# Kernel tuning notes

Hardware: AMD Instinct MI355X
Metric: run time of the kernel (lower is better)

## Reference

```python
import jax, jax.numpy as jnp
import numpy as np

B, TK, H = 32, 1024, 512
N = 2 * H          # hidden_dim * 2
AD = 512           # attention_dimension


def setup_inputs() -> dict:
    key = jax.random.key(0)
    ks = jax.random.split(key, 11)
    s = 0.02  # weight scale
    return {
        's_t_hat': jax.random.normal(ks[0], (B, N), jnp.float32),
        'encoder_outputs': jax.random.normal(ks[1], (B, TK, N), jnp.float32),
        'encoder_feature': jax.random.normal(ks[2], (B * TK, N), jnp.float32),
        'enc_padding_mask': jax.random.uniform(ks[3], (B, TK), jnp.float32),
        'coverage': jax.random.uniform(ks[4], (B, TK), jnp.float32),
        'r_i': jax.random.normal(ks[5], (B, TK, AD), jnp.float32),
        'W_s_w': jax.random.normal(ks[6], (N, N), jnp.float32) * s,
        'W_s_b': jax.random.normal(ks[7], (N,), jnp.float32) * s,
        'W_c_w': jax.random.normal(ks[8], (N, 1), jnp.float32) * s,
        'v_w': jax.random.normal(ks[9], (1, N), jnp.float32) * s,
        'W_r_w': jax.random.normal(ks[10], (N, AD), jnp.float32) * s,
    }


def reference(s_t_hat, encoder_outputs, encoder_feature, enc_padding_mask,
              coverage, r_i, W_s_w, W_s_b, W_c_w, v_w, W_r_w):
    b, t_k, n = encoder_outputs.shape
    # decoder feature: W_s(s_t_hat), broadcast over time
    dec_fea = s_t_hat @ W_s_w.T + W_s_b                       # [b, n]
    enc_feat = encoder_feature.reshape(b, t_k, n)             # [b, t_k, n]
    # coverage feature: W_c applied to scalar coverage per position
    cov_feat = coverage[..., None] * W_c_w[:, 0]              # [b, t_k, n]
    e = jnp.tanh(enc_feat + dec_fea[:, None, :] + cov_feat)   # [b, t_k, n]
    scores = jnp.einsum('btn,n->bt', e, v_w[0])               # [b, t_k]
    attn_ = jax.nn.softmax(scores, axis=1) * enc_padding_mask
    attn = attn_ / attn_.sum(1, keepdims=True)                # renormalized
    c_t = jnp.einsum('bt,btn->bn', attn, encoder_outputs)     # [b, n]
    coverage_new = coverage + attn                            # [b, t_k]
    # structural (LSA) branch
    Wrri = jnp.einsum('bta,na->btn', r_i, W_r_w)              # [b, t_k, n]
    e_s = jnp.tanh(Wrri + dec_fea[:, None, :])
    s2 = jnp.einsum('btn,n->bt', e_s, v_w[0])
    a_struct = (jax.nn.softmax(s2, axis=1) * enc_padding_mask)[:, None, :]  # [b,1,t_k]
    c_t_struct = jnp.einsum('bt,btn->bn', a_struct[:, 0], encoder_outputs)  # [b, n]
    return (c_t, attn, coverage_new, c_t_struct, a_struct)
```

## Files before the change

### kernel.cpp

```cpp
#include <hip/hip_runtime.h>
#include <hip/hip_bf16.h>

static constexpr int BB   = 32;
static constexpr int TKK  = 1024;
static constexpr int ND   = 1024;
static constexpr int ADIM = 512;

typedef __attribute__((ext_vector_type(8))) short bf16x8;
typedef __attribute__((ext_vector_type(4))) float f32x4;

__device__ __forceinline__ float fast_tanh(float x) {
  x = fminf(fmaxf(x, -15.f), 15.f);
  float e = __expf(2.f * x);
  return __fdividef(e - 1.f, e + 1.f);
}

__device__ __forceinline__ short f2bf(float x) {
  unsigned u = __float_as_uint(x);
  u += 0x7FFF + ((u >> 16) & 1);
  return (short)(u >> 16);
}

__device__ __forceinline__ void gload_lds16(const void* g, void* l) {
  __builtin_amdgcn_global_load_lds(
      (const __attribute__((address_space(1))) unsigned int*)g,
      (__attribute__((address_space(3))) unsigned int*)l, 16, 0, 0);
}

__global__ __launch_bounds__(256) void k_cvt2(const float* __restrict__ r_i,
    const float* __restrict__ Wr, short* __restrict__ rb, short* __restrict__ wb) {
  size_t bid = blockIdx.x;
  const float* src;
  short* dst;
  size_t i;
  if (bid < 8192) { src = r_i; dst = rb; i = bid * 256 + threadIdx.x; }
  else            { src = Wr;  dst = wb; i = (bid - 8192) * 256 + threadIdx.x; }
  float4 a = ((const float4*)src)[2 * i];
  float4 b = ((const float4*)src)[2 * i + 1];
  bf16x8 h;
  h[0] = f2bf(a.x); h[1] = f2bf(a.y); h[2] = f2bf(a.z); h[3] = f2bf(a.w);
  h[4] = f2bf(b.x); h[5] = f2bf(b.y); h[6] = f2bf(b.z); h[7] = f2bf(b.w);
  ((bf16x8*)dst)[i] = h;
}

__global__ __launch_bounds__(256) void k_decfea(const float* __restrict__ s_t_hat,
    const float* __restrict__ Wsw, const float* __restrict__ Wsb,
    float* __restrict__ dec) {
  int b  = blockIdx.x >> 3;
  int n0 = (blockIdx.x & 7) << 7;
  int w = threadIdx.x >> 6, lane = threadIdx.x & 63;
  const float4* s4 = (const float4*)(s_t_hat + (size_t)b * ND);
  float4 sv0 = s4[lane], sv1 = s4[lane + 64], sv2 = s4[lane + 128], sv3 = s4[lane + 192];
  for (int nn = 0; nn < 32; nn++) {
    int n = n0 + w * 32 + nn;
    const float4* w4 = (const float4*)(Wsw + (size_t)n * ND);
    float4 wa = w4[lane], wb = w4[lane + 64], wc = w4[lane + 128], wd = w4[lane + 192];
    float acc = sv0.x*wa.x + sv0.y*wa.y + sv0.z*wa.z + sv0.w*wa.w
              + sv1.x*wb.x + sv1.y*wb.y + sv1.z*wb.z + sv1.w*wb.w
              + sv2.x*wc.x + sv2.y*wc.y + sv2.z*wc.z + sv2.w*wc.w
              + sv3.x*wd.x + sv3.y*wd.y + sv3.z*wd.z + sv3.w*wd.w;
    #pragma unroll
    for (int off = 32; off; off >>= 1) acc += __shfl_down(acc, off);
    if (lane == 0) dec[b * ND + n] = acc + Wsb[n];
  }
}

__global__ __launch_bounds__(256) void k_scoresA(const float* __restrict__ ef,
    const float* __restrict__ dec, const float* __restrict__ Wc,
    const float* __restrict__ vw, const float* __restrict__ cov,
    float* __restrict__ scores) {
  const int bt = blockIdx.x * 4 + (threadIdx.x >> 6);
  const int b  = bt >> 10;
  const int lane = threadIdx.x & 63;
  const float c = cov[bt];
  float s = 0.f;
  #pragma unroll
  for (int q = 0; q < 4; ++q) {
    const int col = q * 256 + lane * 4;
    float4 e = *(const float4*)(ef + (size_t)bt * ND + col);
    float4 d = *(const float4*)(dec + (size_t)b * ND + col);
    float4 w = *(const float4*)(Wc + col);
    float4 v = *(const float4*)(vw + col);
    s += v.x * fast_tanh(e.x + d.x + c * w.x)
       + v.y * fast_tanh(e.y + d.y + c * w.y)
       + v.z * fast_tanh(e.z + d.z + c * w.z)
       + v.w * fast_tanh(e.w + d.w + c * w.w);
  }
  #pragma unroll
  for (int off = 32; off; off >>= 1) s += __shfl_down(s, off);
  if (lane == 0) scores[bt] = s;
}

__global__ __launch_bounds__(256) void k_mega(const short* __restrict__ rb,
    const short* __restrict__ wb, const float* __restrict__ dec,
    const float* __restrict__ vw, float* __restrict__ part,
    const float* __restrict__ ef, const float* __restrict__ Wc,
    const float* __restrict__ cov, float* __restrict__ scores) {
  if (blockIdx.x < 2048) {
    __shared__ __align__(16) short As[3][128 * 32];
    __shared__ __align__(16) short Bs[3][128 * 32];
    const int tid = threadIdx.x;
    const int lane = tid & 63, wv = tid >> 6;
    const int wm = wv >> 1, wn = wv & 1;
    const int g = lane >> 4, cl = lane & 15;
    const int bid = blockIdx.x;
    const int swz = (bid & 7) * 256 + (bid >> 3);
    const int mchunk = swz >> 3, nchunk = swz & 7;
    const int b  = mchunk >> 3;
    const int t0 = (mchunk & 7) * 128;
    const int n0 = nchunk * 128;
    const int lrow4 = lane >> 2;
    const int sck   = ((lane & 3) ^ ((lane >> 3) & 3)) * 8;
    const short* Agbase = rb + (size_t)(b * TKK + t0) * ADIM;
    const short* Bgbase = wb + (size_t)n0 * ADIM;
    const int rdsw = (g ^ ((cl >> 1) & 3)) * 8;

    f32x4 acc[4][4];
    #pragma unroll
    for (int m = 0; m < 4; ++m)
      #pragma unroll
      for (int n = 0; n < 4; ++n) acc[m][n] = (f32x4){0.f, 0.f, 0.f, 0.f};

    auto stage = [&](int buf, int kc) {
      const int k0 = kc * 32;
      #pragma unroll
      for (int p = 0; p < 2; ++p) {
        const int rowc = p * 64 + wv * 16;
        const int row  = rowc + lrow4;
        gload_lds16(Agbase + (size_t)row * ADIM + k0 + sck, &As[buf][rowc * 32]);
        gload_lds16(Bgbase + (size_t)row * ADIM + k0 + sck, &Bs[buf][rowc * 32]);
      }
    };

    stage(0, 0);
    stage(1, 1);
    for (int kc = 0; kc < 16; ++kc) {
      if (kc < 14) {
        stage((kc + 2) % 3, kc + 2);
        asm volatile("s_waitcnt vmcnt(8)" ::: "memory");
      } else if (kc == 14) {
        asm volatile("s_waitcnt vmcnt(4)" ::: "memory");
      } else {
        asm volatile("s_waitcnt vmcnt(0)" ::: "memory");
      }
      __builtin_amdgcn_s_barrier();
      const int cur = kc % 3;
      bf16x8 af[4], bfr[4];
      #pragma unroll
      for (int m = 0; m < 4; ++m)
        af[m] = *(const bf16x8*)&As[cur][(wm * 64 + m * 16 + cl) * 32 + rdsw];
      #pragma unroll
      for (int n = 0; n < 4; ++n)
        bfr[n] = *(const bf16x8*)&Bs[cur][(wn * 64 + n * 16 + cl) * 32 + rdsw];
      #pragma unroll
      for (int m = 0; m < 4; ++m)
        #pragma unroll
        for (int n = 0; n < 4; ++n)
          acc[m][n] = __builtin_amdgcn_mfma_f32_16x16x32_bf16(af[m], bfr[n], acc[m][n], 0, 0, 0);
      __builtin_amdgcn_s_barrier();
    }

    float vvv[4], ddd[4];
    #pragma unroll
    for (int n = 0; n < 4; ++n) {
      const int col = n0 + wn * 64 + n * 16 + cl;
      vvv[n] = vw[col];
      ddd[n] = dec[b * ND + col];
    }
    #pragma unroll
    for (int m = 0; m < 4; ++m) {
      #pragma unroll
      for (int r = 0; r < 4; ++r) {
        float s = 0.f;
        #pragma unroll
        for (int n = 0; n < 4; ++n)
          s += vvv[n] * fast_tanh(acc[m][n][r] + ddd[n]);
        #pragma unroll
        for (int off = 1; off < 16; off <<= 1) s += __shfl_xor(s, off);
        if (cl == 0) {
          const int rowg = b * TKK + t0 + wm * 64 + m * 16 + g * 4 + r;
          part[(size_t)rowg * 16 + nchunk * 2 + wn] = s;
        }
      }
    }
  } else {
    const int sbid = blockIdx.x - 2048;
    const int bt0 = sbid * 8 + (threadIdx.x >> 6) * 2;
    const int lane = threadIdx.x & 63;
    const int b0 = bt0 >> 10, b1 = (bt0 + 1) >> 10;
    const float c0 = cov[bt0], c1 = cov[bt0 + 1];
    float s0 = 0.f, s1 = 0.f;
    #pragma unroll
    for (int q = 0; q < 4; ++q) {
      const int col = q * 256 + lane * 4;
      float4 e0 = *(const float4*)(ef + (size_t)bt0 * ND + col);
      float4 e1 = *(const float4*)(ef + (size_t)(bt0 + 1) * ND + col);
      float4 d0 = *(const float4*)(dec + (size_t)b0 * ND + col);
      float4 d1 = *(const float4*)(dec + (size_t)b1 * ND + col);
      float4 w = *(const float4*)(Wc + col);
      float4 v = *(const float4*)(vw + col);
      s0 += v.x * fast_tanh(e0.x + d0.x + c0 * w.x)
          + v.y * fast_tanh(e0.y + d0.y + c0 * w.y)
          + v.z * fast_tanh(e0.z + d0.z + c0 * w.z)
          + v.w * fast_tanh(e0.w + d0.w + c0 * w.w);
      s1 += v.x * fast_tanh(e1.x + d1.x + c1 * w.x)
          + v.y * fast_tanh(e1.y + d1.y + c1 * w.y)
          + v.z * fast_tanh(e1.z + d1.z + c1 * w.z)
          + v.w * fast_tanh(e1.w + d1.w + c1 * w.w);
    }
    #pragma unroll
    for (int off = 32; off; off >>= 1) {
      s0 += __shfl_down(s0, off);
      s1 += __shfl_down(s1, off);
    }
    if (lane == 0) {
      scores[bt0]     = s0;
      scores[bt0 + 1] = s1;
    }
  }
}

__global__ __launch_bounds__(256) void k_gemmB(const float* __restrict__ r_i,
    const float* __restrict__ Wr, const float* __restrict__ dec,
    const float* __restrict__ vw, float* __restrict__ part) {
  __shared__ short As[128 * 64];
  __shared__ short Bs[128 * 64];
  const int tid = threadIdx.x;
  const int lane = tid & 63, wv = tid >> 6;
  const int wm = wv >> 1, wn = wv & 1;
  const int g = lane >> 4, cl = lane & 15;
  const int mchunk = blockIdx.x, nchunk = blockIdx.y;
  const int b  = mchunk >> 3;
  const int t0 = (mchunk & 7) * 128;
  const int n0 = nchunk * 128;
  const float* Ag = r_i + (size_t)(b * TKK + t0) * ADIM;
  const float* Bg = Wr + (size_t)n0 * ADIM;
  const int srow = tid >> 3, skk = (tid & 7) * 8;

  f32x4 acc[4][4];
  #pragma unroll
  for (int m = 0; m < 4; ++m)
    #pragma unroll
    for (int n = 0; n < 4; ++n) acc[m][n] = (f32x4){0.f, 0.f, 0.f, 0.f};

  for (int kc = 0; kc < 8; ++kc) {
    const int k0 = kc * 64;
    __syncthreads();
    #pragma unroll
    for (int dit = 0; dit < 4; ++dit) {
      const int row = dit * 32 + srow;
      const float* sa = Ag + (size_t)row * ADIM + k0 + skk;
      float4 a0 = *(const float4*)sa, a1 = *(const float4*)(sa + 4);
      bf16x8 ha;
      ha[0]=f2bf(a0.x); ha[1]=f2bf(a0.y); ha[2]=f2bf(a0.z); ha[3]=f2bf(a0.w);
      ha[4]=f2bf(a1.x); ha[5]=f2bf(a1.y); ha[6]=f2bf(a1.z); ha[7]=f2bf(a1.w);
      *(bf16x8*)&As[row * 64 + skk] = ha;
      const float* sbp = Bg + (size_t)row * ADIM + k0 + skk;
      float4 b0 = *(const float4*)sbp, b1 = *(const float4*)(sbp + 4);
      bf16x8 hb;
      hb[0]=f2bf(b0.x); hb[1]=f2bf(b0.y); hb[2]=f2bf(b0.z); hb[3]=f2bf(b0.w);
      hb[4]=f2bf(b1.x); hb[5]=f2bf(b1.y); hb[6]=f2bf(b1.z); hb[7]=f2bf(b1.w);
      *(bf16x8*)&Bs[row * 64 + skk] = hb;
    }
    __syncthreads();
    #pragma unroll
    for (int kf = 0; kf < 2; ++kf) {
      bf16x8 af[4], bfr[4];
      #pragma unroll
      for (int m = 0; m < 4; ++m)
        af[m] = *(const bf16x8*)&As[(wm * 64 + m * 16 + cl) * 64 + kf * 32 + g * 8];
      #pragma unroll
      for (int n = 0; n < 4; ++n)
        bfr[n] = *(const bf16x8*)&Bs[(wn * 64 + n * 16 + cl) * 64 + kf * 32 + g * 8];
      #pragma unroll
      for (int m = 0; m < 4; ++m)
        #pragma unroll
        for (int n = 0; n < 4; ++n)
          acc[m][n] = __builtin_amdgcn_mfma_f32_16x16x32_bf16(af[m], bfr[n], acc[m][n], 0, 0, 0);
    }
  }
  float vvv[4], ddd[4];
  #pragma unroll
  for (int n = 0; n < 4; ++n) {
    const int col = n0 + wn * 64 + n * 16 + cl;
    vvv[n] = vw[col];
    ddd[n] = dec[b * ND + col];
  }
  #pragma unroll
  for (int m = 0; m < 4; ++m) {
    #pragma unroll
    for (int r = 0; r < 4; ++r) {
      float s = 0.f;
      #pragma unroll
      for (int n = 0; n < 4; ++n)
        s += vvv[n] * fast_tanh(acc[m][n][r] + ddd[n]);
      #pragma unroll
      for (int off = 1; off < 16; off <<= 1) s += __shfl_xor(s, off);
      if (cl == 0) {
        const int rowg = b * TKK + t0 + wm * 64 + m * 16 + g * 4 + r;
        part[(size_t)rowg * 16 + nchunk * 2 + wn] = s;
      }
    }
  }
}

__global__ __launch_bounds__(256) void k_softmaxAB(const float* __restrict__ scores,
    const float* __restrict__ part, const float* __restrict__ mask,
    const float* __restrict__ cov, float* __restrict__ attn,
    float* __restrict__ covnew, float* __restrict__ astruct) {
  __shared__ float sb[4];
  int tid = threadIdx.x;
  if (blockIdx.x < 32) {
    int b = blockIdx.x;
    float4 s = *(const float4*)(scores + (size_t)b * TKK + tid * 4);
    float m = fmaxf(fmaxf(s.x, s.y), fmaxf(s.z, s.w));
    #pragma unroll
    for (int off = 32; off; off >>= 1) m = fmaxf(m, __shfl_down(m, off));
    if ((tid & 63) == 0) sb[tid >> 6] = m;
    __syncthreads();
    m = fmaxf(fmaxf(sb[0], sb[1]), fmaxf(sb[2], sb[3]));
    float4 mk = *(const float4*)(mask + (size_t)b * TKK + tid * 4);
    float4 e;
    e.x = __expf(s.x - m) * mk.x;
    e.y = __expf(s.y - m) * mk.y;
    e.z = __expf(s.z - m) * mk.z;
    e.w = __expf(s.w - m) * mk.w;
    float sum = e.x + e.y + e.z + e.w;
    #pragma unroll
    for (int off = 32; off; off >>= 1) sum += __shfl_down(sum, off);
    __syncthreads();
    if ((tid & 63) == 0) sb[tid >> 6] = sum;
    __syncthreads();
    float inv = __fdividef(1.f, sb[0] + sb[1] + sb[2] + sb[3]);
    float4 a = {e.x * inv, e.y * inv, e.z * inv, e.w * inv};
    *(float4*)(attn + (size_t)b * TKK + tid * 4) = a;
    float4 c = *(const float4*)(cov + (size_t)b * TKK + tid * 4);
    float4 cn = {c.x + a.x, c.y + a.y, c.z + a.z, c.w + a.w};
    *(float4*)(covnew + (size_t)b * TKK + tid * 4) = cn;
  } else {
    int b = blockIdx.x - 32;
    float sv[4];
    #pragma unroll
    for (int tt = 0; tt < 4; ++tt) {
      const float4* pp = (const float4*)(part + ((size_t)b * TKK + tid * 4 + tt) * 16);
      float4 q0 = pp[0], q1 = pp[1], q2 = pp[2], q3 = pp[3];
      sv[tt] = q0.x+q0.y+q0.z+q0.w + q1.x+q1.y+q1.z+q1.w
             + q2.x+q2.y+q2.z+q2.w + q3.x+q3.y+q3.z+q3.w;
    }
    float m = fmaxf(fmaxf(sv[0], sv[1]), fmaxf(sv[2], sv[3]));
    #pragma unroll
    for (int off = 32; off; off >>= 1) m = fmaxf(m, __shfl_down(m, off));
    if ((tid & 63) == 0) sb[tid >> 6] = m;
    __syncthreads();
    m = fmaxf(fmaxf(sb[0], sb[1]), fmaxf(sb[2], sb[3]));
    float e0 = __expf(sv[0] - m), e1 = __expf(sv[1] - m);
    float e2 = __expf(sv[2] - m), e3 = __expf(sv[3] - m);
    float sum = e0 + e1 + e2 + e3;
    #pragma unroll
    for (int off = 32; off; off >>= 1) sum += __shfl_down(sum, off);
    __syncthreads();
    if ((tid & 63) == 0) sb[tid >> 6] = sum;
    __syncthreads();
    float inv = __fdividef(1.f, sb[0] + sb[1] + sb[2] + sb[3]);
    float4 mk = *(const float4*)(mask + (size_t)b * TKK + tid * 4);
    float4 a = {e0 * mk.x * inv, e1 * mk.y * inv, e2 * mk.z * inv, e3 * mk.w * inv};
    *(float4*)(astruct + (size_t)b * TKK + tid * 4) = a;
  }
}

__global__ __launch_bounds__(256) void k_ctx(const float* __restrict__ enc,
    const float* __restrict__ attn, const float* __restrict__ astr,
    float* __restrict__ partials) {
  int tc = blockIdx.x, b = blockIdx.y;
  int tid = threadIdx.x, lane = tid & 63;
  const float4* e4 = (const float4*)(enc + (size_t)(b * TKK + tc * 32) * ND);
  float a1v = attn[(size_t)b * TKK + tc * 32 + (lane & 31)];
  float a2v = astr[(size_t)b * TKK + tc * 32 + (lane & 31)];
  float4 ac = {0, 0, 0, 0}, as = {0, 0, 0, 0};
  #pragma unroll 8
  for (int m = 0; m < 32; m++) {
    float a1 = __shfl(a1v, m), a2 = __shfl(a2v, m);
    float4 ev = e4[(size_t)m * 256 + tid];
    ac.x += a1 * ev.x; ac.y += a1 * ev.y; ac.z += a1 * ev.z; ac.w += a1 * ev.w;
    as.x += a2 * ev.x; as.y += a2 * ev.y; as.z += a2 * ev.z; as.w += a2 * ev.w;
  }
  float* p = partials + (size_t)(b * 32 + tc) * 2 * ND;
  *(float4*)(p + tid * 4) = ac;
  *(float4*)(p + ND + tid * 4) = as;
}

__global__ __launch_bounds__(256) void k_reduce(const float* __restrict__ partials,
    float* __restrict__ ct, float* __restrict__ cts) {
  int b = blockIdx.x, cx = blockIdx.y;
  int col = cx * 256 + threadIdx.x;
  float sc = 0.f, ss = 0.f;
  for (int tc = 0; tc < 32; tc++) {
    const float* p = partials + (size_t)(b * 32 + tc) * 2 * ND;
    sc += p[col];
    ss += p[ND + col];
  }
  ct[(size_t)b * ND + col] = sc;
  cts[(size_t)b * ND + col] = ss;
}

extern "C" void kernel_launch(void* const* d_in, const int* in_sizes, int n_in,
                              void* d_out, int out_size, void* d_ws, size_t ws_size,
                              hipStream_t stream) {
  const float* s_t_hat = (const float*)d_in[0];
  const float* enc_out  = (const float*)d_in[1];
  const float* enc_feat = (const float*)d_in[2];
  const float* mask     = (const float*)d_in[3];
  const float* cov      = (const float*)d_in[4];
  const float* r_i      = (const float*)d_in[5];
  const float* Wsw      = (const float*)d_in[6];
  const float* Wsb      = (const float*)d_in[7];
  const float* Wc       = (const float*)d_in[8];
  const float* vw       = (const float*)d_in[9];
  const float* Wr       = (const float*)d_in[10];

  float* out    = (float*)d_out;
  float* ct     = out;
  float* attn   = out + 32768;
  float* covnew = out + 65536;
  float* cts    = out + 98304;
  float* astr   = out + 131072;

  float* ws       = (float*)d_ws;
  float* dec      = ws;
  float* scores   = ws + 32768;
  float* s2part   = ws + 65536;
  float* partials = ws + 589824;
  short* rb       = (short*)(ws + 2686976);
  short* wb       = rb + 16777216;
  const size_t NEEDED = 2686976ull * 4 + 16777216ull * 2 + 524288ull * 2;

  k_decfea<<<256, 256, 0, stream>>>(s_t_hat, Wsw, Wsb, dec);
  if (ws_size >= NEEDED) {
    k_cvt2<<<8448, 256, 0, stream>>>(r_i, Wr, rb, wb);
    k_mega<<<6144, 256, 0, stream>>>(rb, wb, dec, vw, s2part,
                                     enc_feat, Wc, cov, scores);
  } else {
    k_scoresA<<<8192, 256, 0, stream>>>(enc_feat, dec, Wc, vw, cov, scores);
    k_gemmB<<<dim3(256, 8), 256, 0, stream>>>(r_i, Wr, dec, vw, s2part);
  }
  k_softmaxAB<<<64, 256, 0, stream>>>(scores, s2part, mask, cov, attn, covnew, astr);
  k_ctx<<<dim3(32, BB), 256, 0, stream>>>(enc_out, attn, astr, partials);
  k_reduce<<<dim3(BB, 4), 256, 0, stream>>>(partials, ct, cts);
}
```

Measured before the change: 163.1 us.

## Fuse dec_fea into conversion kernel and interleave GEMM with score blocks

```diff
diff --git a/kernel.cpp b/kernel.cpp
--- a/kernel.cpp
+++ b/kernel.cpp
@@ -27,20 +27,43 @@
       (__attribute__((address_space(3))) unsigned int*)l, 16, 0, 0);
 }
 
-__global__ __launch_bounds__(256) void k_cvt2(const float* __restrict__ r_i,
-    const float* __restrict__ Wr, short* __restrict__ rb, short* __restrict__ wb) {
+__global__ __launch_bounds__(256) void k_pre(const float* __restrict__ r_i,
+    const float* __restrict__ Wr, short* __restrict__ rb, short* __restrict__ wb,
+    const float* __restrict__ s_t_hat, const float* __restrict__ Wsw,
+    const float* __restrict__ Wsb, float* __restrict__ dec) {
   size_t bid = blockIdx.x;
-  const float* src;
-  short* dst;
-  size_t i;
-  if (bid < 8192) { src = r_i; dst = rb; i = bid * 256 + threadIdx.x; }
-  else            { src = Wr;  dst = wb; i = (bid - 8192) * 256 + threadIdx.x; }
-  float4 a = ((const float4*)src)[2 * i];
-  float4 b = ((const float4*)src)[2 * i + 1];
-  bf16x8 h;
-  h[0] = f2bf(a.x); h[1] = f2bf(a.y); h[2] = f2bf(a.z); h[3] = f2bf(a.w);
-  h[4] = f2bf(b.x); h[5] = f2bf(b.y); h[6] = f2bf(b.z); h[7] = f2bf(b.w);
-  ((bf16x8*)dst)[i] = h;
+  if (bid < 8448) {
+    const float* src;
+    short* dst;
+    size_t i;
+    if (bid < 8192) { src = r_i; dst = rb; i = bid * 256 + threadIdx.x; }
+    else            { src = Wr;  dst = wb; i = (bid - 8192) * 256 + threadIdx.x; }
+    float4 a = ((const float4*)src)[2 * i];
+    float4 b = ((const float4*)src)[2 * i + 1];
+    bf16x8 h;
+    h[0] = f2bf(a.x); h[1] = f2bf(a.y); h[2] = f2bf(a.z); h[3] = f2bf(a.w);
+    h[4] = f2bf(b.x); h[5] = f2bf(b.y); h[6] = f2bf(b.z); h[7] = f2bf(b.w);
+    ((bf16x8*)dst)[i] = h;
+  } else {
+    int db = (int)bid - 8448;
+    int b  = db >> 3;
+    int n0 = (db & 7) << 7;
+    int w = threadIdx.x >> 6, lane = threadIdx.x & 63;
+    const float4* s4 = (const float4*)(s_t_hat + (size_t)b * ND);
+    float4 sv0 = s4[lane], sv1 = s4[lane + 64], sv2 = s4[lane + 128], sv3 = s4[lane + 192];
+    for (int nn = 0; nn < 32; nn++) {
+      int n = n0 + w * 32 + nn;
+      const float4* w4 = (const float4*)(Wsw + (size_t)n * ND);
+      float4 wa = w4[lane], wb2 = w4[lane + 64], wc = w4[lane + 128], wd = w4[lane + 192];
+      float acc = sv0.x*wa.x + sv0.y*wa.y + sv0.z*wa.z + sv0.w*wa.w
+                + sv1.x*wb2.x + sv1.y*wb2.y + sv1.z*wb2.z + sv1.w*wb2.w
+                + sv2.x*wc.x + sv2.y*wc.y + sv2.z*wc.z + sv2.w*wc.w
+                + sv3.x*wd.x + sv3.y*wd.y + sv3.z*wd.z + sv3.w*wd.w;
+      #pragma unroll
+      for (int off = 32; off; off >>= 1) acc += __shfl_down(acc, off);
+      if (lane == 0) dec[b * ND + n] = acc + Wsb[n];
+    }
+  }
 }
 
 __global__ __launch_bounds__(256) void k_decfea(const float* __restrict__ s_t_hat,
@@ -96,15 +119,16 @@
     const float* __restrict__ vw, float* __restrict__ part,
     const float* __restrict__ ef, const float* __restrict__ Wc,
     const float* __restrict__ cov, float* __restrict__ scores) {
-  if (blockIdx.x < 2048) {
-    __shared__ __align__(16) short As[3][128 * 32];
-    __shared__ __align__(16) short Bs[3][128 * 32];
+  const int r3 = blockIdx.x % 3;
+  const int g3 = blockIdx.x / 3;
+  if (r3 == 0) {
+    __shared__ __align__(16) short As[2][128 * 32];
+    __shared__ __align__(16) short Bs[2][128 * 32];
     const int tid = threadIdx.x;
     const int lane = tid & 63, wv = tid >> 6;
     const int wm = wv >> 1, wn = wv & 1;
     const int g = lane >> 4, cl = lane & 15;
-    const int bid = blockIdx.x;
-    const int swz = (bid & 7) * 256 + (bid >> 3);
+    const int swz = (g3 & 7) * 256 + (g3 >> 3);
     const int mchunk = swz >> 3, nchunk = swz & 7;
     const int b  = mchunk >> 3;
     const int t0 = (mchunk & 7) * 128;
@@ -133,18 +157,15 @@
     };
 
     stage(0, 0);
-    stage(1, 1);
     for (int kc = 0; kc < 16; ++kc) {
-      if (kc < 14) {
-        stage((kc + 2) % 3, kc + 2);
-        asm volatile("s_waitcnt vmcnt(8)" ::: "memory");
-      } else if (kc == 14) {
+      const int cur = kc & 1;
+      if (kc < 15) {
+        stage(cur ^ 1, kc + 1);
         asm volatile("s_waitcnt vmcnt(4)" ::: "memory");
       } else {
         asm volatile("s_waitcnt vmcnt(0)" ::: "memory");
       }
       __builtin_amdgcn_s_barrier();
-      const int cur = kc % 3;
       bf16x8 af[4], bfr[4];
       #pragma unroll
       for (int m = 0; m < 4; ++m)
@@ -184,8 +205,8 @@
       }
     }
   } else {
-    const int sbid = blockIdx.x - 2048;
-    const int bt0 = sbid * 8 + (threadIdx.x >> 6) * 2;
+    const int sidx = 2 * g3 + (r3 - 1);
+    const int bt0 = sidx * 8 + (threadIdx.x >> 6) * 2;
     const int lane = threadIdx.x & 63;
     const int b0 = bt0 >> 10, b1 = (bt0 + 1) >> 10;
     const float c0 = cov[bt0], c1 = cov[bt0 + 1];
@@ -434,12 +455,12 @@
   short* wb       = rb + 16777216;
   const size_t NEEDED = 2686976ull * 4 + 16777216ull * 2 + 524288ull * 2;
 
-  k_decfea<<<256, 256, 0, stream>>>(s_t_hat, Wsw, Wsb, dec);
   if (ws_size >= NEEDED) {
-    k_cvt2<<<8448, 256, 0, stream>>>(r_i, Wr, rb, wb);
+    k_pre<<<8704, 256, 0, stream>>>(r_i, Wr, rb, wb, s_t_hat, Wsw, Wsb, dec);
     k_mega<<<6144, 256, 0, stream>>>(rb, wb, dec, vw, s2part,
                                      enc_feat, Wc, cov, scores);
   } else {
+    k_decfea<<<256, 256, 0, stream>>>(s_t_hat, Wsw, Wsb, dec);
     k_scoresA<<<8192, 256, 0, stream>>>(enc_feat, dec, Wc, vw, cov, scores);
     k_gemmB<<<dim3(256, 8), 256, 0, stream>>>(r_i, Wr, dec, vw, s2part);
   }
```

Measured after the change: 164.0 us. Within noise of the previous version (+0.6%).
